# Kernel tuning notes

Hardware: AMD Instinct MI355X
Metric: run time of the kernel (lower is better)

## Reference

```python
import jax, jax.numpy as jnp
import numpy as np

B, C, O, H, W = 16, 256, 256, 64, 64
T_DIM, E, K = 512, 4, 3


def setup_inputs() -> dict:
    key = jax.random.key(0)
    ks = jax.random.split(key, 12)
    def rn(k, shape, s=0.02):
        return jax.random.normal(k, shape, jnp.float32) * s
    return dict(
        x=jax.random.normal(ks[0], (B, C, H, W), jnp.float32),
        time_emb=jax.random.normal(ks[1], (B, T_DIM), jnp.float32),
        Wq=rn(ks[2], (C, T_DIM)), bq=jnp.zeros((C,), jnp.float32),
        Wk=rn(ks[3], (C, C)), bk=jnp.zeros((C,), jnp.float32),
        Wv=rn(ks[4], (C, C)), bv=jnp.zeros((C,), jnp.float32),
        Wm1=rn(ks[5], (C // 4, C)), bm1=jnp.zeros((C // 4,), jnp.float32),
        Wm2=rn(ks[6], (C, C // 4)), bm2=jnp.zeros((C,), jnp.float32),
        Wc=rn(ks[7], (E, C)), bc=jnp.zeros((E,), jnp.float32),
        expert_w=rn(ks[8], (E, O, C, K, K), s=0.05),  # [E, O, C_in/groups, K, K]
        expert_b=rn(ks[9], (E, O), s=0.05),
    )


def reference(x, time_emb, Wq, bq, Wk, bk, Wv, bv, Wm1, bm1, Wm2, bm2, Wc, bc, expert_w, expert_b):
    # --- router (eval mode: no gating noise) ---
    pooled = x.mean(axis=(2, 3))                      # [B, C] == avg_pool over full HxW
    q = time_emb @ Wq.T + bq                          # [B, C]
    k = pooled @ Wk.T + bk                            # [B, C]
    attn = jax.nn.sigmoid(q * k)
    v = pooled @ Wv.T + bv
    x_att = v * attn
    h = jax.nn.gelu(x_att @ Wm1.T + bm1, approximate=False) @ Wm2.T + bm2
    x_mix = x_att + h
    logits = x_mix @ Wc.T + bc                        # [B, E]
    rw = jnp.tanh(logits)                             # routing weights [B, E]

    # --- per-sample expert-weight mixing ---
    w_eff = jnp.einsum('be,eoihw->boihw', rw, expert_w)  # [B, O, C, K, K]
    b_eff = rw @ expert_b                                 # [B, O]

    # --- per-sample conv (equivalent to groups=B trick) ---
    def conv_one(xb, wb):
        # xb: [C, H, W], wb: [O, C, K, K]
        return jax.lax.conv_general_dilated(
            xb[None], wb, window_strides=(1, 1), padding=[(1, 1), (1, 1)],
            dimension_numbers=('NCHW', 'OIHW', 'NCHW'))[0]

    out = jax.vmap(conv_one)(x, w_eff)                 # [B, O, H, W]
    return out + b_eff[:, :, None, None]
```

## Files before the change

kernel.cpp:

```cpp
#include <hip/hip_runtime.h>

typedef __bf16 bf16x8 __attribute__((ext_vector_type(8)));
typedef float f32x4 __attribute__((ext_vector_type(4)));

__device__ __forceinline__ unsigned short f2bf(float f) {
  union { float f; unsigned int u; } v;
  v.f = f;
  unsigned int r = v.u + 0x7FFFu + ((v.u >> 16) & 1u);
  return (unsigned short)(r >> 16);
}

__device__ __forceinline__ void load_lds16(const void* g, void* l) {
  __builtin_amdgcn_global_load_lds(
      (__attribute__((address_space(1))) void*)(void*)g,
      (__attribute__((address_space(3))) void*)l, 16, 0, 0);
}

__global__ void transpose_kernel(const float* __restrict__ x, unsigned short* __restrict__ xTpad,
                                 float* __restrict__ part) {
  int bid = blockIdx.x;
  int b = bid / 66, hp = bid % 66;
  unsigned short* rowbase = xTpad + ((size_t)(b * 66 + hp)) * 66 * 256;
  int t = threadIdx.x;
  if (hp == 0 || hp == 65) {
    uint4 z = make_uint4(0u, 0u, 0u, 0u);
    for (int i = t; i < 2112; i += 256) ((uint4*)rowbase)[i] = z;
    return;
  }
  int h = hp - 1;
  __shared__ unsigned short lds[64][264];
  __shared__ float psum[256];
  const float* xb = x + ((size_t)b * 256 * 64 + h) * 64;
  int lane = t & 63;
  #pragma unroll
  for (int g = 0; g < 16; ++g) {
    int c = g * 16 + (t >> 4);
    int w0 = (t & 15) * 4;
    float4 v = *(const float4*)&xb[(size_t)c * 4096 + w0];
    lds[w0 + 0][c] = f2bf(v.x);
    lds[w0 + 1][c] = f2bf(v.y);
    lds[w0 + 2][c] = f2bf(v.z);
    lds[w0 + 3][c] = f2bf(v.w);
    float s = v.x + v.y + v.z + v.w;
    s += __shfl_xor(s, 1); s += __shfl_xor(s, 2);
    s += __shfl_xor(s, 4); s += __shfl_xor(s, 8);
    if ((lane & 15) == 0) psum[c] = s;
  }
  __syncthreads();
  #pragma unroll
  for (int p = 0; p < 8; ++p) {
    int w = p * 8 + (t >> 5);
    int seg = t & 31;
    uint4 u = *(const uint4*)&lds[w][seg * 8];
    *(uint4*)&rowbase[(w + 1) * 256 + seg * 8] = u;
  }
  if (t < 64) {
    uint4 z = make_uint4(0u, 0u, 0u, 0u);
    int row = (t >> 5) ? 65 : 0;
    *(uint4*)&rowbase[row * 256 + (t & 31) * 8] = z;
  }
  if (t < 256) part[((size_t)b * 64 + h) * 256 + t] = psum[t];
}

__global__ void router_kernel(
    const float* __restrict__ time_emb, const float* __restrict__ part,
    const float* __restrict__ Wq, const float* __restrict__ bq,
    const float* __restrict__ Wk, const float* __restrict__ bk,
    const float* __restrict__ Wv, const float* __restrict__ bv,
    const float* __restrict__ Wm1, const float* __restrict__ bm1,
    const float* __restrict__ Wm2, const float* __restrict__ bm2,
    const float* __restrict__ Wc, const float* __restrict__ bc,
    const float* __restrict__ expert_b,
    float* __restrict__ rw_out, float* __restrict__ beff_out) {
  int b = blockIdx.x, t = threadIdx.x;
  __shared__ float te[512], pl[256], xa[256], m1s[64], xms[256], rws[4];
  te[t] = time_emb[b * 512 + t];
  te[t + 256] = time_emb[b * 512 + 256 + t];
  {
    float s = 0.f;
    const float* pp = part + (size_t)b * 16384 + t;
    for (int hh = 0; hh < 64; ++hh) s += pp[hh * 256];
    pl[t] = s * (1.0f / 4096.0f);
  }
  __syncthreads();
  float q = bq[t], k = bk[t], v = bv[t];
  const float4* wq4 = (const float4*)(Wq + (size_t)t * 512);
  #pragma unroll 4
  for (int i = 0; i < 128; ++i) {
    float4 w4 = wq4[i];
    q += w4.x * te[i*4] + w4.y * te[i*4+1] + w4.z * te[i*4+2] + w4.w * te[i*4+3];
  }
  const float4* wk4 = (const float4*)(Wk + (size_t)t * 256);
  const float4* wv4 = (const float4*)(Wv + (size_t)t * 256);
  #pragma unroll 4
  for (int i = 0; i < 64; ++i) {
    float4 a4 = wk4[i], b4 = wv4[i];
    float p0 = pl[i*4], p1 = pl[i*4+1], p2 = pl[i*4+2], p3 = pl[i*4+3];
    k += a4.x * p0 + a4.y * p1 + a4.z * p2 + a4.w * p3;
    v += b4.x * p0 + b4.y * p1 + b4.z * p2 + b4.w * p3;
  }
  float attn = 1.0f / (1.0f + expf(-(q * k)));
  float xatt = v * attn;
  xa[t] = xatt;
  __syncthreads();
  if (t < 64) {
    float s = bm1[t];
    const float4* w1 = (const float4*)(Wm1 + (size_t)t * 256);
    #pragma unroll 4
    for (int i = 0; i < 64; ++i) {
      float4 w4 = w1[i];
      s += w4.x * xa[i*4] + w4.y * xa[i*4+1] + w4.z * xa[i*4+2] + w4.w * xa[i*4+3];
    }
    m1s[t] = 0.5f * s * (1.0f + erff(s * 0.7071067811865476f));
  }
  __syncthreads();
  float hsum = bm2[t];
  const float* w2 = Wm2 + (size_t)t * 64;
  for (int j = 0; j < 64; ++j) hsum += m1s[j] * w2[j];
  float xm = xatt + hsum;
  xms[t] = xm;
  __syncthreads();
  if (t < 4) {
    float s = bc[t];
    const float* wc = Wc + (size_t)t * 256;
    for (int i = 0; i < 256; ++i) s += xms[i] * wc[i];
    float r = tanhf(s);
    rws[t] = r;
    rw_out[b * 4 + t] = r;
  }
  __syncthreads();
  float be = 0.f;
  #pragma unroll
  for (int e = 0; e < 4; ++e) be += rws[e] * expert_b[e * 256 + t];
  beff_out[b * 256 + t] = be;
}

__global__ void wmix_kernel(const float* __restrict__ ew, const float* __restrict__ rw,
                            unsigned short* __restrict__ wmix) {
  int o = blockIdx.x, t = threadIdx.x;
  __shared__ float lew[4][2304];
  __shared__ float rsh[64];
  if (t < 64) rsh[t] = rw[t];
  #pragma unroll
  for (int e = 0; e < 4; ++e) {
    const float* s = ew + ((size_t)e * 256 + o) * 2304;
    #pragma unroll
    for (int j = 0; j < 9; ++j) lew[e][j * 256 + t] = s[j * 256 + t];
  }
  __syncthreads();
  float wv[4][9];
  #pragma unroll
  for (int e = 0; e < 4; ++e)
    #pragma unroll
    for (int tt = 0; tt < 9; ++tt) wv[e][tt] = lew[e][t * 9 + tt];
  for (int b = 0; b < 16; ++b) {
    float r0 = rsh[b*4], r1 = rsh[b*4+1], r2 = rsh[b*4+2], r3 = rsh[b*4+3];
    unsigned short* wo = wmix + ((size_t)b * 256 + o) * 2304 + t;
    #pragma unroll
    for (int tt = 0; tt < 9; ++tt) {
      float m = r0 * wv[0][tt] + r1 * wv[1][tt] + r2 * wv[2][tt] + r3 * wv[3][tt];
      wo[tt * 256] = f2bf(m);
    }
  }
}

__global__ __launch_bounds__(512, 2) void conv_kernel(
    const unsigned short* __restrict__ xT, const unsigned short* __restrict__ wmix,
    const float* __restrict__ beff, float* __restrict__ out) {
  __shared__ unsigned short As[2][16384];
  __shared__ unsigned short Bs[2][16384];
  int bid = blockIdx.x;
  int b = ((bid & 7) << 1) | ((bid >> 7) & 1);
  int nt = (bid >> 3) & 15;
  int h0 = nt << 2;
  int tid = threadIdx.x;
  int wid = tid >> 6, lane = tid & 63;
  int lm = lane & 15, lg = lane >> 4;
  int wm = wid >> 1, wn = wid & 1;

  const unsigned short* wmb = wmix + (size_t)b * 256 * 2304;
  const unsigned short* xTb = xT + (size_t)b * 66 * 66 * 256;

  int lr = lane >> 3;
  int slot_g = (lane & 7) ^ lr;
  int a_lane = lr * 2304 + slot_g * 8;
  int b_lane = lr * 256 + slot_g * 8;

  int sw0 = ((0 + lg) ^ (lm & 7)) * 8;
  int sw1 = ((4 + lg) ^ (lm & 7)) * 8;

  auto stA = [&](int buf, int s, int u) {
    const unsigned short* src = wmb + (size_t)(u * 64 + wid * 8) * 2304 + s * 64 + a_lane;
    load_lds16(src, &As[buf][(u * 64 + wid * 8) * 64]);
  };
  auto stB = [&](int buf, int s, int bh, int rq) {
    int tap = s >> 2;
    int kh = tap / 3, kw = tap - kh * 3;
    int c0 = (s & 3) * 64;
    const unsigned short* src =
        xTb + (size_t)((h0 + bh * 2 + rq + kh) * 66 + wid * 8 + kw) * 256 + c0 + b_lane;
    load_lds16(src, &Bs[buf][(bh * 128 + rq * 64 + wid * 8) * 64]);
  };

  f32x4 acc[4][8];
  #pragma unroll
  for (int mf = 0; mf < 4; ++mf)
    #pragma unroll
    for (int nf = 0; nf < 8; ++nf)
      acc[mf][nf] = (f32x4){0.f, 0.f, 0.f, 0.f};

  stA(0, 0, 0); stA(0, 0, 1); stA(0, 0, 2); stA(0, 0, 3);
  stB(0, 0, 0, 0); stB(0, 0, 1, 0);
  stB(0, 0, 0, 1); stB(0, 0, 1, 1);
  asm volatile("s_waitcnt vmcnt(2)" ::: "memory");
  __builtin_amdgcn_s_barrier();

  auto do_tile = [&](int t, int BUF) __attribute__((always_inline)) {
    bool st = (t < 35);
    int s = t + 1;
    bf16x8 a01[2][2], a23[2][2], bA[4][2], bB[4][2];
    #pragma unroll
    for (int mf = 0; mf < 2; ++mf) {
      a01[mf][0] = *(const bf16x8*)&As[BUF][(wm * 64 + mf * 16 + lm) * 64 + sw0];
      a01[mf][1] = *(const bf16x8*)&As[BUF][(wm * 64 + mf * 16 + lm) * 64 + sw1];
    }
    #pragma unroll
    for (int nf = 0; nf < 4; ++nf) {
      bA[nf][0] = *(const bf16x8*)&Bs[BUF][(wn * 128 + nf * 16 + lm) * 64 + sw0];
      bA[nf][1] = *(const bf16x8*)&Bs[BUF][(wn * 128 + nf * 16 + lm) * 64 + sw1];
    }
    if (st) { stA(BUF ^ 1, s, 0); stA(BUF ^ 1, s, 1); stA(BUF ^ 1, s, 2); }
    __builtin_amdgcn_s_barrier();
    asm volatile("s_waitcnt lgkmcnt(0)" ::: "memory");
    __builtin_amdgcn_sched_barrier(0);
    __builtin_amdgcn_s_setprio(1);
    #pragma unroll
    for (int mf = 0; mf < 2; ++mf)
      #pragma unroll
      for (int nf = 0; nf < 4; ++nf)
        #pragma unroll
        for (int kk = 0; kk < 2; ++kk)
          acc[mf][nf] = __builtin_amdgcn_mfma_f32_16x16x32_bf16(a01[mf][kk], bA[nf][kk], acc[mf][nf], 0, 0, 0);
    __builtin_amdgcn_s_setprio(0);
    __builtin_amdgcn_s_barrier();
    #pragma unroll
    for (int mf = 0; mf < 2; ++mf) {
      a23[mf][0] = *(const bf16x8*)&As[BUF][(wm * 64 + (mf + 2) * 16 + lm) * 64 + sw0];
      a23[mf][1] = *(const bf16x8*)&As[BUF][(wm * 64 + (mf + 2) * 16 + lm) * 64 + sw1];
    }
    if (st) { stA(BUF ^ 1, s, 3); stB(BUF ^ 1, s, 0, 0); stB(BUF ^ 1, s, 1, 0); }
    if (st) { asm volatile("s_waitcnt vmcnt(6)" ::: "memory"); }
    else    { asm volatile("s_waitcnt vmcnt(0)" ::: "memory"); }
    __builtin_amdgcn_s_barrier();
    asm volatile("s_waitcnt lgkmcnt(0)" ::: "memory");
    __builtin_amdgcn_sched_barrier(0);
    __builtin_amdgcn_s_setprio(1);
    #pragma unroll
    for (int mf = 0; mf < 2; ++mf)
      #pragma unroll
      for (int nf = 0; nf < 4; ++nf)
        #pragma unroll
        for (int kk = 0; kk < 2; ++kk)
          acc[mf + 2][nf] = __builtin_amdgcn_mfma_f32_16x16x32_bf16(a23[mf][kk], bA[nf][kk], acc[mf + 2][nf], 0, 0, 0);
    __builtin_amdgcn_s_setprio(0);
    __builtin_amdgcn_s_barrier();
    #pragma unroll
    for (int nf = 0; nf < 4; ++nf) {
      bB[nf][0] = *(const bf16x8*)&Bs[BUF][(wn * 128 + 64 + nf * 16 + lm) * 64 + sw0];
      bB[nf][1] = *(const bf16x8*)&Bs[BUF][(wn * 128 + 64 + nf * 16 + lm) * 64 + sw1];
    }
    if (st) stB(BUF ^ 1, s, 0, 1);
    __builtin_amdgcn_s_barrier();
    asm volatile("s_waitcnt lgkmcnt(0)" ::: "memory");
    __builtin_amdgcn_sched_barrier(0);
    __builtin_amdgcn_s_setprio(1);
    #pragma unroll
    for (int mf = 0; mf < 2; ++mf)
      #pragma unroll
      for (int nf = 0; nf < 4; ++nf)
        #pragma unroll
        for (int kk = 0; kk < 2; ++kk)
          acc[mf + 2][nf + 4] = __builtin_amdgcn_mfma_f32_16x16x32_bf16(a23[mf][kk], bB[nf][kk], acc[mf + 2][nf + 4], 0, 0, 0);
    __builtin_amdgcn_s_setprio(0);
    __builtin_amdgcn_s_barrier();
    if (st) stB(BUF ^ 1, s, 1, 1);
    asm volatile("s_waitcnt vmcnt(2)" ::: "memory");
    __builtin_amdgcn_s_barrier();
    __builtin_amdgcn_s_setprio(1);
    #pragma unroll
    for (int mf = 0; mf < 2; ++mf)
      #pragma unroll
      for (int nf = 0; nf < 4; ++nf)
        #pragma unroll
        for (int kk = 0; kk < 2; ++kk)
          acc[mf][nf + 4] = __builtin_amdgcn_mfma_f32_16x16x32_bf16(a01[mf][kk], bB[nf][kk], acc[mf][nf + 4], 0, 0, 0);
    __builtin_amdgcn_s_setprio(0);
    __builtin_amdgcn_s_barrier();
  };

  for (int th = 0; th < 18; ++th) {
    do_tile(2 * th, 0);
    do_tile(2 * th + 1, 1);
  }

  #pragma unroll
  for (int mf = 0; mf < 4; ++mf) {
    int o = wm * 64 + mf * 16 + lg * 4;
    float be0 = beff[b * 256 + o + 0];
    float be1 = beff[b * 256 + o + 1];
    float be2 = beff[b * 256 + o + 2];
    float be3 = beff[b * 256 + o + 3];
    #pragma unroll
    for (int nf = 0; nf < 8; ++nf) {
      int n = wn * 128 + nf * 16 + lm;
      int hh = h0 + (n >> 6), w = n & 63;
      float* op = out + (((size_t)(b * 256 + o)) * 64 + hh) * 64 + w;
      op[0]            = acc[mf][nf][0] + be0;
      op[4096]         = acc[mf][nf][1] + be1;
      op[2 * 4096]     = acc[mf][nf][2] + be2;
      op[3 * 4096]     = acc[mf][nf][3] + be3;
    }
  }
}

extern "C" void kernel_launch(void* const* d_in, const int* in_sizes, int n_in,
                              void* d_out, int out_size, void* d_ws, size_t ws_size,
                              hipStream_t stream) {
  const float* x        = (const float*)d_in[0];
  const float* time_emb = (const float*)d_in[1];
  const float* Wq = (const float*)d_in[2];
  const float* bq = (const float*)d_in[3];
  const float* Wk = (const float*)d_in[4];
  const float* bk = (const float*)d_in[5];
  const float* Wv = (const float*)d_in[6];
  const float* bv = (const float*)d_in[7];
  const float* Wm1 = (const float*)d_in[8];
  const float* bm1 = (const float*)d_in[9];
  const float* Wm2 = (const float*)d_in[10];
  const float* bm2 = (const float*)d_in[11];
  const float* Wc = (const float*)d_in[12];
  const float* bc = (const float*)d_in[13];
  const float* expert_w = (const float*)d_in[14];
  const float* expert_b = (const float*)d_in[15];
  float* out = (float*)d_out;

  char* ws = (char*)d_ws;
  float* rw   = (float*)(ws + 0);
  float* beff = (float*)(ws + 1024);
  float* part = (float*)(ws + 20480);
  unsigned short* xTpad = (unsigned short*)(ws + 1069056);
  unsigned short* wmix  = (unsigned short*)(ws + 1069056 + 35684352);

  transpose_kernel<<<1056, 256, 0, stream>>>(x, xTpad, part);
  router_kernel<<<16, 256, 0, stream>>>(time_emb, part, Wq, bq, Wk, bk, Wv, bv,
                                        Wm1, bm1, Wm2, bm2, Wc, bc, expert_b, rw, beff);
  wmix_kernel<<<256, 256, 0, stream>>>(expert_w, rw, wmix);
  conv_kernel<<<256, 512, 0, stream>>>(xTpad, wmix, beff, out);
}
```

Before: 148.0 us.

## Issue all next-tile conv loads up front and split router GEMVs across 512 threads

In the conv kernel, all global-to-LDS loads for the next K tile are now issued at the first phase instead of being spread across the four MFMA phases. The vmcnt waits and the barrier structure change to match, which removes one barrier per tile. The goal is to give memory more time to overlap with compute, at the cost of more outstanding loads and a later wait point. Separately, the router kernel runs with 512 threads so the q projection and the k/v projections run on different thread halves in parallel, shortening its serial GEMV chain.

```diff
diff --git a/kernel.cpp b/kernel.cpp
--- a/kernel.cpp
+++ b/kernel.cpp
@@ -72,67 +72,81 @@
     const float* __restrict__ Wc, const float* __restrict__ bc,
     const float* __restrict__ expert_b,
     float* __restrict__ rw_out, float* __restrict__ beff_out) {
-  int b = blockIdx.x, t = threadIdx.x;
-  __shared__ float te[512], pl[256], xa[256], m1s[64], xms[256], rws[4];
-  te[t] = time_emb[b * 512 + t];
-  te[t + 256] = time_emb[b * 512 + 256 + t];
-  {
+  int b = blockIdx.x, tid = threadIdx.x;
+  int t = tid & 255;
+  __shared__ float te[512], pl[256], qs[256], xa[256], m1s[64], xms[256], rws[4];
+  te[tid] = time_emb[b * 512 + tid];
+  if (tid < 256) {
     float s = 0.f;
-    const float* pp = part + (size_t)b * 16384 + t;
+    const float* pp = part + (size_t)b * 16384 + tid;
     for (int hh = 0; hh < 64; ++hh) s += pp[hh * 256];
-    pl[t] = s * (1.0f / 4096.0f);
-  }
-  __syncthreads();
-  float q = bq[t], k = bk[t], v = bv[t];
-  const float4* wq4 = (const float4*)(Wq + (size_t)t * 512);
-  #pragma unroll 4
-  for (int i = 0; i < 128; ++i) {
-    float4 w4 = wq4[i];
-    q += w4.x * te[i*4] + w4.y * te[i*4+1] + w4.z * te[i*4+2] + w4.w * te[i*4+3];
-  }
-  const float4* wk4 = (const float4*)(Wk + (size_t)t * 256);
-  const float4* wv4 = (const float4*)(Wv + (size_t)t * 256);
-  #pragma unroll 4
-  for (int i = 0; i < 64; ++i) {
-    float4 a4 = wk4[i], b4 = wv4[i];
-    float p0 = pl[i*4], p1 = pl[i*4+1], p2 = pl[i*4+2], p3 = pl[i*4+3];
-    k += a4.x * p0 + a4.y * p1 + a4.z * p2 + a4.w * p3;
-    v += b4.x * p0 + b4.y * p1 + b4.z * p2 + b4.w * p3;
-  }
-  float attn = 1.0f / (1.0f + expf(-(q * k)));
-  float xatt = v * attn;
-  xa[t] = xatt;
-  __syncthreads();
-  if (t < 64) {
-    float s = bm1[t];
-    const float4* w1 = (const float4*)(Wm1 + (size_t)t * 256);
+    pl[tid] = s * (1.0f / 4096.0f);
+  }
+  __syncthreads();
+  if (tid < 256) {
+    float q = bq[t];
+    const float4* wq4 = (const float4*)(Wq + (size_t)t * 512);
+    #pragma unroll 4
+    for (int i = 0; i < 128; ++i) {
+      float4 w4 = wq4[i];
+      q += w4.x * te[i*4] + w4.y * te[i*4+1] + w4.z * te[i*4+2] + w4.w * te[i*4+3];
+    }
+    qs[t] = q;
+  } else {
+    float k = bk[t], v = bv[t];
+    const float4* wk4 = (const float4*)(Wk + (size_t)t * 256);
+    const float4* wv4 = (const float4*)(Wv + (size_t)t * 256);
+    #pragma unroll 4
+    for (int i = 0; i < 64; ++i) {
+      float4 a4 = wk4[i], b4 = wv4[i];
+      float p0 = pl[i*4], p1 = pl[i*4+1], p2 = pl[i*4+2], p3 = pl[i*4+3];
+      k += a4.x * p0 + a4.y * p1 + a4.z * p2 + a4.w * p3;
+      v += b4.x * p0 + b4.y * p1 + b4.z * p2 + b4.w * p3;
+    }
+    xa[t] = k;
+    xms[t] = v;
+  }
+  __syncthreads();
+  if (tid < 256) {
+    float k = xa[t], v = xms[t];
+    float attn = 1.0f / (1.0f + expf(-(qs[t] * k)));
+    float xatt = v * attn;
+    qs[t] = xatt;
+  }
+  __syncthreads();
+  if (tid < 64) {
+    float s = bm1[tid];
+    const float4* w1 = (const float4*)(Wm1 + (size_t)tid * 256);
     #pragma unroll 4
     for (int i = 0; i < 64; ++i) {
       float4 w4 = w1[i];
-      s += w4.x * xa[i*4] + w4.y * xa[i*4+1] + w4.z * xa[i*4+2] + w4.w * xa[i*4+3];
-    }
-    m1s[t] = 0.5f * s * (1.0f + erff(s * 0.7071067811865476f));
-  }
-  __syncthreads();
-  float hsum = bm2[t];
-  const float* w2 = Wm2 + (size_t)t * 64;
-  for (int j = 0; j < 64; ++j) hsum += m1s[j] * w2[j];
-  float xm = xatt + hsum;
-  xms[t] = xm;
-  __syncthreads();
-  if (t < 4) {
-    float s = bc[t];
-    const float* wc = Wc + (size_t)t * 256;
+      s += w4.x * qs[i*4] + w4.y * qs[i*4+1] + w4.z * qs[i*4+2] + w4.w * qs[i*4+3];
+    }
+    m1s[tid] = 0.5f * s * (1.0f + erff(s * 0.7071067811865476f));
+  }
+  __syncthreads();
+  if (tid < 256) {
+    float hsum = bm2[t];
+    const float* w2 = Wm2 + (size_t)t * 64;
+    for (int j = 0; j < 64; ++j) hsum += m1s[j] * w2[j];
+    xms[t] = qs[t] + hsum;
+  }
+  __syncthreads();
+  if (tid < 4) {
+    float s = bc[tid];
+    const float* wc = Wc + (size_t)tid * 256;
     for (int i = 0; i < 256; ++i) s += xms[i] * wc[i];
     float r = tanhf(s);
-    rws[t] = r;
-    rw_out[b * 4 + t] = r;
-  }
-  __syncthreads();
-  float be = 0.f;
-  #pragma unroll
-  for (int e = 0; e < 4; ++e) be += rws[e] * expert_b[e * 256 + t];
-  beff_out[b * 256 + t] = be;
+    rws[tid] = r;
+    rw_out[b * 4 + tid] = r;
+  }
+  __syncthreads();
+  if (tid < 256) {
+    float be = 0.f;
+    #pragma unroll
+    for (int e = 0; e < 4; ++e) be += rws[e] * expert_b[e * 256 + t];
+    beff_out[b * 256 + t] = be;
+  }
 }
 
 __global__ void wmix_kernel(const float* __restrict__ ew, const float* __restrict__ rw,
@@ -229,7 +243,11 @@
       bA[nf][0] = *(const bf16x8*)&Bs[BUF][(wn * 128 + nf * 16 + lm) * 64 + sw0];
       bA[nf][1] = *(const bf16x8*)&Bs[BUF][(wn * 128 + nf * 16 + lm) * 64 + sw1];
     }
-    if (st) { stA(BUF ^ 1, s, 0); stA(BUF ^ 1, s, 1); stA(BUF ^ 1, s, 2); }
+    if (st) {
+      stA(BUF ^ 1, s, 0); stA(BUF ^ 1, s, 1); stA(BUF ^ 1, s, 2); stA(BUF ^ 1, s, 3);
+      stB(BUF ^ 1, s, 0, 0); stB(BUF ^ 1, s, 1, 0);
+      stB(BUF ^ 1, s, 0, 1); stB(BUF ^ 1, s, 1, 1);
+    }
     __builtin_amdgcn_s_barrier();
     asm volatile("s_waitcnt lgkmcnt(0)" ::: "memory");
     __builtin_amdgcn_sched_barrier(0);
@@ -248,8 +266,7 @@
       a23[mf][0] = *(const bf16x8*)&As[BUF][(wm * 64 + (mf + 2) * 16 + lm) * 64 + sw0];
       a23[mf][1] = *(const bf16x8*)&As[BUF][(wm * 64 + (mf + 2) * 16 + lm) * 64 + sw1];
     }
-    if (st) { stA(BUF ^ 1, s, 3); stB(BUF ^ 1, s, 0, 0); stB(BUF ^ 1, s, 1, 0); }
-    if (st) { asm volatile("s_waitcnt vmcnt(6)" ::: "memory"); }
+    if (st) { asm volatile("s_waitcnt vmcnt(8)" ::: "memory"); }
     else    { asm volatile("s_waitcnt vmcnt(0)" ::: "memory"); }
     __builtin_amdgcn_s_barrier();
     asm volatile("s_waitcnt lgkmcnt(0)" ::: "memory");
@@ -269,7 +286,6 @@
       bB[nf][0] = *(const bf16x8*)&Bs[BUF][(wn * 128 + 64 + nf * 16 + lm) * 64 + sw0];
       bB[nf][1] = *(const bf16x8*)&Bs[BUF][(wn * 128 + 64 + nf * 16 + lm) * 64 + sw1];
     }
-    if (st) stB(BUF ^ 1, s, 0, 1);
     __builtin_amdgcn_s_barrier();
     asm volatile("s_waitcnt lgkmcnt(0)" ::: "memory");
     __builtin_amdgcn_sched_barrier(0);
@@ -283,9 +299,6 @@
           acc[mf + 2][nf + 4] = __builtin_amdgcn_mfma_f32_16x16x32_bf16(a23[mf][kk], bB[nf][kk], acc[mf + 2][nf + 4], 0, 0, 0);
     __builtin_amdgcn_s_setprio(0);
     __builtin_amdgcn_s_barrier();
-    if (st) stB(BUF ^ 1, s, 1, 1);
-    asm volatile("s_waitcnt vmcnt(2)" ::: "memory");
-    __builtin_amdgcn_s_barrier();
     __builtin_amdgcn_s_setprio(1);
     #pragma unroll
     for (int mf = 0; mf < 2; ++mf)
@@ -295,6 +308,8 @@
         for (int kk = 0; kk < 2; ++kk)
           acc[mf][nf + 4] = __builtin_amdgcn_mfma_f32_16x16x32_bf16(a01[mf][kk], bB[nf][kk], acc[mf][nf + 4], 0, 0, 0);
     __builtin_amdgcn_s_setprio(0);
+    if (st) { asm volatile("s_waitcnt vmcnt(2)" ::: "memory"); }
+    else    { asm volatile("s_waitcnt vmcnt(0)" ::: "memory"); }
     __builtin_amdgcn_s_barrier();
   };
 
@@ -352,7 +367,7 @@
   unsigned short* wmix  = (unsigned short*)(ws + 1069056 + 35684352);
 
   transpose_kernel<<<1056, 256, 0, stream>>>(x, xTpad, part);
-  router_kernel<<<16, 256, 0, stream>>>(time_emb, part, Wq, bq, Wk, bk, Wv, bv,
+  router_kernel<<<16, 512, 0, stream>>>(time_emb, part, Wq, bq, Wk, bk, Wv, bv,
                                         Wm1, bm1, Wm2, bm2, Wc, bc, expert_b, rw, beff);
   wmix_kernel<<<256, 256, 0, stream>>>(expert_w, rw, wmix);
   conv_kernel<<<256, 512, 0, stream>>>(xTpad, wmix, beff, out);
```

Result: slower. 152.6 us (+3.1%).
